# Kernel optimization log

Measured on AMD Instinct MI355X. Metric: run time of the kernel, lower is better.

## Reference

```python
import jax, jax.numpy as jnp
import numpy as np
import math

TEXT_EMBEDDING_DIM = 768.0
SEQ = 81
DIM = 64
B, H = 256, 16


def setup_inputs() -> dict:
    key = jax.random.key(0)
    kq, kk, kv, ke = jax.random.split(key, 4)
    Q = jax.random.normal(kq, (B, H, SEQ, DIM), dtype=jnp.float32)
    K = jax.random.normal(kk, (B, H, SEQ, DIM), dtype=jnp.float32)
    V = jax.random.normal(kv, (B, H, SEQ, DIM), dtype=jnp.float32)
    emb_table = jax.random.normal(ke, (2 * SEQ + 1, DIM), dtype=jnp.float32)
    return {"Q": Q, "K": K, "V": V, "emb_table": emb_table, "use_causal": 1}


def reference(Q, K, V, emb_table, use_causal):
    S = Q.shape[-2]
    # relative index matrix: rel[i, j] = (S - 1 + i) - j, in [0, 2S-2]
    rel = jnp.arange(S - 1, 2 * S - 1)[:, None] - jnp.arange(S)  # [S, S] int
    emb = emb_table[rel]  # [S, S, d]
    # QK^T plus learned relative-position bias
    eij = jnp.einsum('bhid,bhjd->bhij', Q, K) + jnp.einsum('bhid,ijd->bhij', Q, emb)
    attn = eij / math.sqrt(TEXT_EMBEDDING_DIM)  # note: sqrt(768), not sqrt(dim), per source
    if use_causal:
        i = jnp.arange(S)[:, None]
        j = jnp.arange(S)
        mask = jnp.where(i >= j, 0.0, -1000000000.0).astype(attn.dtype)  # [S, S]
        attn = attn + mask
    attn = jax.nn.softmax(attn, axis=-1)
    return jnp.einsum('bhij,bhjd->bhid', attn, V)
```

## Files before the change

kernel.cpp:

```cpp
#include <hip/hip_runtime.h>
#include <hip/hip_bf16.h>

#define SEQ 81
#define DIM 64
#define NT  384
#define NW  6
#define LDK 68
#define LDV 100
#define LDP 100

typedef short bf16x8 __attribute__((ext_vector_type(8)));
typedef short bf16x4 __attribute__((ext_vector_type(4)));
typedef float f32x4  __attribute__((ext_vector_type(4)));

static constexpr float kS2 = 0.0520587716f;

__device__ __forceinline__ short f2bf(float f) {
    __hip_bfloat16 h = __float2bfloat16(f);
    return __builtin_bit_cast(short, h);
}
__device__ __forceinline__ float bf2f(short h) {
    unsigned u = ((unsigned)(unsigned short)h) << 16;
    return __builtin_bit_cast(float, u);
}
__device__ __forceinline__ bf16x8 cat8(bf16x4 a, bf16x4 b) {
    bf16x8 r;
    r[0]=a[0]; r[1]=a[1]; r[2]=a[2]; r[3]=a[3];
    r[4]=b[0]; r[5]=b[1]; r[6]=b[2]; r[7]=b[3];
    return r;
}

__global__ void emb_cvt_kernel(const float* __restrict__ in, short* __restrict__ out, int n) {
    int i = blockIdx.x * 256 + threadIdx.x;
    if (i < n) out[i] = f2bf(in[i]);
}

__global__ __launch_bounds__(NT, 8)
void rpsa_kernel(const float* __restrict__ Q, const float* __restrict__ K,
                 const float* __restrict__ V, const short* __restrict__ embw,
                 const int* __restrict__ ucp, float* __restrict__ out)
{
    extern __shared__ char smraw[];
    short* sVt = (short*)smraw;
    short* sK  = (short*)(smraw + 12800);
    short* sP  = (short*)(smraw + 12800);

    const int tid = threadIdx.x;
    const size_t base = (size_t)blockIdx.x * (SEQ * DIM);
    const int uc = ucp[0];
    const int w  = tid >> 6, L = tid & 63;
    const int lr = L & 15,  lg = L >> 4;
    const int iRow = 16*w + lr;

    bf16x8 aq0, aq1;
    {
        const int qrow = (iRow < SEQ) ? iRow : (SEQ - 1);
        const float* qp = Q + base + qrow*DIM + 8*lg;
        const f32x4 q0 = *(const f32x4*)(qp);
        const f32x4 q1 = *(const f32x4*)(qp + 4);
        const f32x4 q2 = *(const f32x4*)(qp + 32);
        const f32x4 q3 = *(const f32x4*)(qp + 36);
        #pragma unroll
        for (int t = 0; t < 4; ++t) {
            aq0[t]   = f2bf(q0[t]*kS2);
            aq0[4+t] = f2bf(q1[t]*kS2);
            aq1[t]   = f2bf(q2[t]*kS2);
            aq1[4+t] = f2bf(q3[t]*kS2);
        }
    }

    for (int u = tid; u < 96 * DIM / 8; u += NT) {
        const int row = u >> 3, so = (u & 7) * 8;
        bf16x4 lo = {0,0,0,0}, hi = {0,0,0,0};
        if (row < SEQ) {
            const f32x4 k0 = *(const f32x4*)(K + base + row*DIM + so);
            const f32x4 k1 = *(const f32x4*)(K + base + row*DIM + so + 4);
            #pragma unroll
            for (int t = 0; t < 4; ++t) { lo[t] = f2bf(k0[t]); hi[t] = f2bf(k1[t]); }
        }
        *(bf16x4*)(sK + row*LDK + so)     = lo;
        *(bf16x4*)(sK + row*LDK + so + 4) = hi;
    }
    {
        const int j4 = tid >> 4;
        const int d4 = tid & 15;
        f32x4 rw[4];
        #pragma unroll
        for (int e = 0; e < 4; ++e) {
            const int j = 4*j4 + e;
            rw[e] = (j < SEQ) ? *(const f32x4*)(V + base + j*DIM + 4*d4)
                              : (f32x4){0.f,0.f,0.f,0.f};
        }
        #pragma unroll
        for (int c = 0; c < 4; ++c) {
            const int d = 4*d4 + c;
            bf16x4 pv = { f2bf(rw[0][c]), f2bf(rw[1][c]), f2bf(rw[2][c]), f2bf(rw[3][c]) };
            *(bf16x4*)(sVt + d*LDV + 4*j4) = pv;
        }
    }

    bf16x4 qe[NW];
    #pragma unroll
    for (int nt2 = 0; nt2 < NW; ++nt2) {
        if (nt2 > w) continue;
        int erow = 80 + 16*nt2 + lr;
        if (erow > 2*SEQ) erow = 2*SEQ;
        bf16x8 e0 = *(const bf16x8*)(embw + erow*DIM + 8*lg);
        bf16x8 e1 = *(const bf16x8*)(embw + erow*DIM + 32 + 8*lg);
        f32x4 a = {0.f,0.f,0.f,0.f};
        a = __builtin_amdgcn_mfma_f32_16x16x32_bf16(e0, aq0, a, 0, 0, 0);
        a = __builtin_amdgcn_mfma_f32_16x16x32_bf16(e1, aq1, a, 0, 0, 0);
        bf16x4 p = { f2bf(a[0]), f2bf(a[1]), f2bf(a[2]), f2bf(a[3]) };
        qe[nt2] = p;
    }
    __syncthreads();

    f32x4 accs[NW] = {};
    const int ntEnd = uc ? w : (NW - 1);
    #pragma unroll
    for (int nt = 0; nt < NW; ++nt) {
        if (nt > ntEnd) continue;
        const int kr = 16*nt + lr;
        bf16x8 b0 = cat8(*(const bf16x4*)(sK + kr*LDK + 8*lg),
                         *(const bf16x4*)(sK + kr*LDK + 8*lg + 4));
        bf16x8 b1 = cat8(*(const bf16x4*)(sK + kr*LDK + 32 + 8*lg),
                         *(const bf16x4*)(sK + kr*LDK + 32 + 8*lg + 4));
        f32x4 a = accs[nt];
        a = __builtin_amdgcn_mfma_f32_16x16x32_bf16(b0, aq0, a, 0, 0, 0);
        a = __builtin_amdgcn_mfma_f32_16x16x32_bf16(b1, aq1, a, 0, 0, 0);
        accs[nt] = a;
    }
    __syncthreads();

    #pragma unroll
    for (int nt2 = 0; nt2 < NW; ++nt2) {
        if (nt2 > w) continue;
        #pragma unroll
        for (int r = 0; r < 4; ++r) {
            const int j = 16*(w - nt2) + lr - 4*lg - r;
            if (j >= 0) sP[iRow*LDP + j] = qe[nt2][r];
        }
    }
    if (!uc) {
        #pragma unroll
        for (int nt2 = 0; nt2 < NW - 1; ++nt2) {
            if (nt2 < w) continue;
            const int erow = 16*nt2 + lr;
            bf16x8 e0 = *(const bf16x8*)(embw + erow*DIM + 8*lg);
            bf16x8 e1 = *(const bf16x8*)(embw + erow*DIM + 32 + 8*lg);
            f32x4 a = {0.f,0.f,0.f,0.f};
            a = __builtin_amdgcn_mfma_f32_16x16x32_bf16(e0, aq0, a, 0, 0, 0);
            a = __builtin_amdgcn_mfma_f32_16x16x32_bf16(e1, aq1, a, 0, 0, 0);
            #pragma unroll
            for (int r = 0; r < 4; ++r) {
                const int rel = 16*nt2 + 4*lg + r;
                if (rel >= iRow) sP[iRow*LDP + (80 + iRow - rel)] = f2bf(a[r]);
            }
        }
    }

    const int jmax = uc ? ((iRow < SEQ-1) ? iRow : SEQ-1) : (SEQ-1);
    float sum = 0.f;
    #pragma unroll
    for (int nt = 0; nt < NW; ++nt) {
        short* slot = sP + iRow*LDP + 16*nt + 4*lg;
        if (nt <= ntEnd) {
            bf16x4 bias = *(const bf16x4*)(slot);
            bf16x4 p;
            #pragma unroll
            for (int r = 0; r < 4; ++r) {
                const int j = 16*nt + 4*lg + r;
                const float x = accs[nt][r] + bf2f(bias[r]);
                const float e = (j <= jmax) ? exp2f(x) : 0.f;
                sum += e;
                p[r] = f2bf(e);
            }
            *(bf16x4*)(slot) = p;
        } else {
            *(bf16x4*)(slot) = (bf16x4){0,0,0,0};
        }
    }
    sum += __shfl_xor(sum, 16);
    sum += __shfl_xor(sum, 32);
    const float inv = 1.f / sum;

    bf16x8 ap0, ap1, ap2;
    {
        ap0 = cat8(*(const bf16x4*)(sP + iRow*LDP + 8*lg),
                   *(const bf16x4*)(sP + iRow*LDP + 8*lg + 4));
        ap1 = cat8(*(const bf16x4*)(sP + iRow*LDP + 32 + 8*lg),
                   *(const bf16x4*)(sP + iRow*LDP + 32 + 8*lg + 4));
        ap2 = cat8(*(const bf16x4*)(sP + iRow*LDP + 64 + 8*lg),
                   *(const bf16x4*)(sP + iRow*LDP + 64 + 8*lg + 4));
    }
    #pragma unroll
    for (int nt = 0; nt < 4; ++nt) {
        const int d = 16*nt + lr;
        bf16x8 b0 = cat8(*(const bf16x4*)(sVt + d*LDV + 8*lg),
                         *(const bf16x4*)(sVt + d*LDV + 8*lg + 4));
        bf16x8 b1 = cat8(*(const bf16x4*)(sVt + d*LDV + 32 + 8*lg),
                         *(const bf16x4*)(sVt + d*LDV + 32 + 8*lg + 4));
        bf16x8 b2 = cat8(*(const bf16x4*)(sVt + d*LDV + 64 + 8*lg),
                         *(const bf16x4*)(sVt + d*LDV + 64 + 8*lg + 4));
        f32x4 a = {0.f,0.f,0.f,0.f};
        a = __builtin_amdgcn_mfma_f32_16x16x32_bf16(b0, ap0, a, 0, 0, 0);
        a = __builtin_amdgcn_mfma_f32_16x16x32_bf16(b1, ap1, a, 0, 0, 0);
        a = __builtin_amdgcn_mfma_f32_16x16x32_bf16(b2, ap2, a, 0, 0, 0);
        if (iRow < SEQ) {
            f32x4 o = { a[0]*inv, a[1]*inv, a[2]*inv, a[3]*inv };
            *(f32x4*)(out + base + iRow*DIM + 16*nt + 4*lg) = o;
        }
    }
}

extern "C" void kernel_launch(void* const* d_in, const int* in_sizes, int n_in,
                              void* d_out, int out_size, void* d_ws, size_t ws_size,
                              hipStream_t stream) {
    const float* Q   = (const float*)d_in[0];
    const float* K   = (const float*)d_in[1];
    const float* V   = (const float*)d_in[2];
    const float* emb = (const float*)d_in[3];
    const int*   uc  = (const int*)d_in[4];
    float* out = (float*)d_out;

    const int nbh   = in_sizes[0] / (SEQ * DIM);
    const int n_emb = in_sizes[3];

    short* embw = (short*)d_ws;
    emb_cvt_kernel<<<(n_emb + 255) / 256, 256, 0, stream>>>(emb, embw, n_emb);

    const size_t smem = 32000;
    hipFuncSetAttribute(reinterpret_cast<const void*>(rpsa_kernel),
                        hipFuncAttributeMaxDynamicSharedMemorySize, (int)smem);
    rpsa_kernel<<<nbh, NT, smem, stream>>>(Q, K, V, embw, uc, out);
}
```

Before: 83.85 us.

## Load K directly into MFMA registers, drop K smem staging and a barrier

K is now read from global memory straight into MFMA operand registers and converted to bf16 in registers, instead of being staged through shared memory. This removes the K staging loop and one of the two __syncthreads. sP gets its own shared-memory region, LDV/LDP padding becomes 102, and bias scores are written to sP as soon as they are computed. The PV stage also skips k-slices above the causal limit for each wave. The tradeoff is that K rows are loaded redundantly by different waves, which adds global/L2 traffic in exchange for less LDS work and synchronisation.

```diff
diff --git a/kernel.cpp b/kernel.cpp
--- a/kernel.cpp
+++ b/kernel.cpp
@@ -5,9 +5,8 @@
 #define DIM 64
 #define NT  384
 #define NW  6
-#define LDK 68
-#define LDV 100
-#define LDP 100
+#define LDV 102
+#define LDP 102
 
 typedef short bf16x8 __attribute__((ext_vector_type(8)));
 typedef short bf16x4 __attribute__((ext_vector_type(4)));
@@ -42,8 +41,7 @@
 {
     extern __shared__ char smraw[];
     short* sVt = (short*)smraw;
-    short* sK  = (short*)(smraw + 12800);
-    short* sP  = (short*)(smraw + 12800);
+    short* sP  = (short*)(smraw + 13056);
 
     const int tid = threadIdx.x;
     const size_t base = (size_t)blockIdx.x * (SEQ * DIM);
@@ -51,6 +49,24 @@
     const int w  = tid >> 6, L = tid & 63;
     const int lr = L & 15,  lg = L >> 4;
     const int iRow = 16*w + lr;
+
+    {
+        const int j4 = tid >> 4;
+        const int d4 = tid & 15;
+        f32x4 rw[4];
+        #pragma unroll
+        for (int e = 0; e < 4; ++e) {
+            const int j = 4*j4 + e;
+            rw[e] = (j < SEQ) ? *(const f32x4*)(V + base + j*DIM + 4*d4)
+                              : (f32x4){0.f,0.f,0.f,0.f};
+        }
+        #pragma unroll
+        for (int c = 0; c < 4; ++c) {
+            const int d = 4*d4 + c;
+            bf16x4 pv = { f2bf(rw[0][c]), f2bf(rw[1][c]), f2bf(rw[2][c]), f2bf(rw[3][c]) };
+            *(bf16x4*)(sVt + d*LDV + 4*j4) = pv;
+        }
+    }
 
     bf16x8 aq0, aq1;
     {
@@ -69,37 +85,6 @@
         }
     }
 
-    for (int u = tid; u < 96 * DIM / 8; u += NT) {
-        const int row = u >> 3, so = (u & 7) * 8;
-        bf16x4 lo = {0,0,0,0}, hi = {0,0,0,0};
-        if (row < SEQ) {
-            const f32x4 k0 = *(const f32x4*)(K + base + row*DIM + so);
-            const f32x4 k1 = *(const f32x4*)(K + base + row*DIM + so + 4);
-            #pragma unroll
-            for (int t = 0; t < 4; ++t) { lo[t] = f2bf(k0[t]); hi[t] = f2bf(k1[t]); }
-        }
-        *(bf16x4*)(sK + row*LDK + so)     = lo;
-        *(bf16x4*)(sK + row*LDK + so + 4) = hi;
-    }
-    {
-        const int j4 = tid >> 4;
-        const int d4 = tid & 15;
-        f32x4 rw[4];
-        #pragma unroll
-        for (int e = 0; e < 4; ++e) {
-            const int j = 4*j4 + e;
-            rw[e] = (j < SEQ) ? *(const f32x4*)(V + base + j*DIM + 4*d4)
-                              : (f32x4){0.f,0.f,0.f,0.f};
-        }
-        #pragma unroll
-        for (int c = 0; c < 4; ++c) {
-            const int d = 4*d4 + c;
-            bf16x4 pv = { f2bf(rw[0][c]), f2bf(rw[1][c]), f2bf(rw[2][c]), f2bf(rw[3][c]) };
-            *(bf16x4*)(sVt + d*LDV + 4*j4) = pv;
-        }
-    }
-
-    bf16x4 qe[NW];
     #pragma unroll
     for (int nt2 = 0; nt2 < NW; ++nt2) {
         if (nt2 > w) continue;
@@ -110,35 +95,10 @@
         f32x4 a = {0.f,0.f,0.f,0.f};
         a = __builtin_amdgcn_mfma_f32_16x16x32_bf16(e0, aq0, a, 0, 0, 0);
         a = __builtin_amdgcn_mfma_f32_16x16x32_bf16(e1, aq1, a, 0, 0, 0);
-        bf16x4 p = { f2bf(a[0]), f2bf(a[1]), f2bf(a[2]), f2bf(a[3]) };
-        qe[nt2] = p;
-    }
-    __syncthreads();
-
-    f32x4 accs[NW] = {};
-    const int ntEnd = uc ? w : (NW - 1);
-    #pragma unroll
-    for (int nt = 0; nt < NW; ++nt) {
-        if (nt > ntEnd) continue;
-        const int kr = 16*nt + lr;
-        bf16x8 b0 = cat8(*(const bf16x4*)(sK + kr*LDK + 8*lg),
-                         *(const bf16x4*)(sK + kr*LDK + 8*lg + 4));
-        bf16x8 b1 = cat8(*(const bf16x4*)(sK + kr*LDK + 32 + 8*lg),
-                         *(const bf16x4*)(sK + kr*LDK + 32 + 8*lg + 4));
-        f32x4 a = accs[nt];
-        a = __builtin_amdgcn_mfma_f32_16x16x32_bf16(b0, aq0, a, 0, 0, 0);
-        a = __builtin_amdgcn_mfma_f32_16x16x32_bf16(b1, aq1, a, 0, 0, 0);
-        accs[nt] = a;
-    }
-    __syncthreads();
-
-    #pragma unroll
-    for (int nt2 = 0; nt2 < NW; ++nt2) {
-        if (nt2 > w) continue;
         #pragma unroll
         for (int r = 0; r < 4; ++r) {
             const int j = 16*(w - nt2) + lr - 4*lg - r;
-            if (j >= 0) sP[iRow*LDP + j] = qe[nt2][r];
+            if (j >= 0) sP[iRow*LDP + j] = f2bf(a[r]);
         }
     }
     if (!uc) {
@@ -157,6 +117,30 @@
                 if (rel >= iRow) sP[iRow*LDP + (80 + iRow - rel)] = f2bf(a[r]);
             }
         }
+    }
+
+    f32x4 accs[NW] = {};
+    const int ntEnd = uc ? w : (NW - 1);
+    #pragma unroll
+    for (int nt = 0; nt < NW; ++nt) {
+        if (nt > ntEnd) continue;
+        const int kr0 = 16*nt + lr;
+        const int kr  = (kr0 < SEQ) ? kr0 : (SEQ - 1);
+        const float* kp = K + base + kr*DIM + 8*lg;
+        const f32x4 k0 = *(const f32x4*)(kp);
+        const f32x4 k1 = *(const f32x4*)(kp + 4);
+        const f32x4 k2 = *(const f32x4*)(kp + 32);
+        const f32x4 k3 = *(const f32x4*)(kp + 36);
+        bf16x8 b0, b1;
+        #pragma unroll
+        for (int t = 0; t < 4; ++t) {
+            b0[t] = f2bf(k0[t]); b0[4+t] = f2bf(k1[t]);
+            b1[t] = f2bf(k2[t]); b1[4+t] = f2bf(k3[t]);
+        }
+        f32x4 a = accs[nt];
+        a = __builtin_amdgcn_mfma_f32_16x16x32_bf16(b0, aq0, a, 0, 0, 0);
+        a = __builtin_amdgcn_mfma_f32_16x16x32_bf16(b1, aq1, a, 0, 0, 0);
+        accs[nt] = a;
     }
 
     const int jmax = uc ? ((iRow < SEQ-1) ? iRow : SEQ-1) : (SEQ-1);
@@ -184,28 +168,33 @@
     sum += __shfl_xor(sum, 32);
     const float inv = 1.f / sum;
 
+    __syncthreads();
+
+    const int nks = uc ? ((w >> 1) + 1) : 3;
     bf16x8 ap0, ap1, ap2;
-    {
-        ap0 = cat8(*(const bf16x4*)(sP + iRow*LDP + 8*lg),
-                   *(const bf16x4*)(sP + iRow*LDP + 8*lg + 4));
-        ap1 = cat8(*(const bf16x4*)(sP + iRow*LDP + 32 + 8*lg),
-                   *(const bf16x4*)(sP + iRow*LDP + 32 + 8*lg + 4));
-        ap2 = cat8(*(const bf16x4*)(sP + iRow*LDP + 64 + 8*lg),
-                   *(const bf16x4*)(sP + iRow*LDP + 64 + 8*lg + 4));
-    }
+    ap0 = cat8(*(const bf16x4*)(sP + iRow*LDP + 8*lg),
+               *(const bf16x4*)(sP + iRow*LDP + 8*lg + 4));
+    ap1 = cat8(*(const bf16x4*)(sP + iRow*LDP + 32 + 8*lg),
+               *(const bf16x4*)(sP + iRow*LDP + 32 + 8*lg + 4));
+    ap2 = cat8(*(const bf16x4*)(sP + iRow*LDP + 64 + 8*lg),
+               *(const bf16x4*)(sP + iRow*LDP + 64 + 8*lg + 4));
     #pragma unroll
     for (int nt = 0; nt < 4; ++nt) {
         const int d = 16*nt + lr;
+        f32x4 a = {0.f,0.f,0.f,0.f};
         bf16x8 b0 = cat8(*(const bf16x4*)(sVt + d*LDV + 8*lg),
                          *(const bf16x4*)(sVt + d*LDV + 8*lg + 4));
-        bf16x8 b1 = cat8(*(const bf16x4*)(sVt + d*LDV + 32 + 8*lg),
-                         *(const bf16x4*)(sVt + d*LDV + 32 + 8*lg + 4));
-        bf16x8 b2 = cat8(*(const bf16x4*)(sVt + d*LDV + 64 + 8*lg),
-                         *(const bf16x4*)(sVt + d*LDV + 64 + 8*lg + 4));
-        f32x4 a = {0.f,0.f,0.f,0.f};
         a = __builtin_amdgcn_mfma_f32_16x16x32_bf16(b0, ap0, a, 0, 0, 0);
-        a = __builtin_amdgcn_mfma_f32_16x16x32_bf16(b1, ap1, a, 0, 0, 0);
-        a = __builtin_amdgcn_mfma_f32_16x16x32_bf16(b2, ap2, a, 0, 0, 0);
+        if (nks > 1) {
+            bf16x8 b1 = cat8(*(const bf16x4*)(sVt + d*LDV + 32 + 8*lg),
+                             *(const bf16x4*)(sVt + d*LDV + 32 + 8*lg + 4));
+            a = __builtin_amdgcn_mfma_f32_16x16x32_bf16(b1, ap1, a, 0, 0, 0);
+        }
+        if (nks > 2) {
+            bf16x8 b2 = cat8(*(const bf16x4*)(sVt + d*LDV + 64 + 8*lg),
+                             *(const bf16x4*)(sVt + d*LDV + 64 + 8*lg + 4));
+            a = __builtin_amdgcn_mfma_f32_16x16x32_bf16(b2, ap2, a, 0, 0, 0);
+        }
         if (iRow < SEQ) {
             f32x4 o = { a[0]*inv, a[1]*inv, a[2]*inv, a[3]*inv };
             *(f32x4*)(out + base + iRow*DIM + 16*nt + 4*lg) = o;
@@ -229,7 +218,7 @@
     short* embw = (short*)d_ws;
     emb_cvt_kernel<<<(n_emb + 255) / 256, 256, 0, stream>>>(emb, embw, n_emb);
 
-    const size_t smem = 32000;
+    const size_t smem = 32640;
     hipFuncSetAttribute(reinterpret_cast<const void*>(rpsa_kernel),
                         hipFuncAttributeMaxDynamicSharedMemorySize, (int)smem);
     rpsa_kernel<<<nbh, NT, smem, stream>>>(Q, K, V, embw, uc, out);
```

Measured after the change: 150.9 us. +80.0%, slower.

## Fuse embedding conversion into main kernel and skip masked PV k-steps

Applied to the files above, without the earlier changes.

Removes the separate fp32-to-bf16 embedding conversion kernel and launch; the attention kernel now reads fp32 embedding rows directly and converts them in registers. Under causal masking, each wave skips the PV MFMA k-slices (and their LDS loads) that lie entirely in the masked region. The V and P LDS row strides change from 100 to 102, presumably to reduce bank conflicts, which makes shared memory slightly larger. In exchange, each block does redundant embedding conversion and twice as many global bytes per embedding load, and there is a wave-dependent branch.

```diff
diff --git a/kernel.cpp b/kernel.cpp
--- a/kernel.cpp
+++ b/kernel.cpp
@@ -6,8 +6,8 @@
 #define NT  384
 #define NW  6
 #define LDK 68
-#define LDV 100
-#define LDP 100
+#define LDV 102
+#define LDP 102
 
 typedef short bf16x8 __attribute__((ext_vector_type(8)));
 typedef short bf16x4 __attribute__((ext_vector_type(4)));
@@ -29,21 +29,22 @@
     r[4]=b[0]; r[5]=b[1]; r[6]=b[2]; r[7]=b[3];
     return r;
 }
-
-__global__ void emb_cvt_kernel(const float* __restrict__ in, short* __restrict__ out, int n) {
-    int i = blockIdx.x * 256 + threadIdx.x;
-    if (i < n) out[i] = f2bf(in[i]);
+__device__ __forceinline__ bf16x8 cvt8(f32x4 a, f32x4 b) {
+    bf16x8 r;
+    #pragma unroll
+    for (int t = 0; t < 4; ++t) { r[t] = f2bf(a[t]); r[4+t] = f2bf(b[t]); }
+    return r;
 }
 
 __global__ __launch_bounds__(NT, 8)
 void rpsa_kernel(const float* __restrict__ Q, const float* __restrict__ K,
-                 const float* __restrict__ V, const short* __restrict__ embw,
+                 const float* __restrict__ V, const float* __restrict__ emb,
                  const int* __restrict__ ucp, float* __restrict__ out)
 {
     extern __shared__ char smraw[];
     short* sVt = (short*)smraw;
-    short* sK  = (short*)(smraw + 12800);
-    short* sP  = (short*)(smraw + 12800);
+    short* sK  = (short*)(smraw + 13056);
+    short* sP  = (short*)(smraw + 13056);
 
     const int tid = threadIdx.x;
     const size_t base = (size_t)blockIdx.x * (SEQ * DIM);
@@ -56,17 +57,8 @@
     {
         const int qrow = (iRow < SEQ) ? iRow : (SEQ - 1);
         const float* qp = Q + base + qrow*DIM + 8*lg;
-        const f32x4 q0 = *(const f32x4*)(qp);
-        const f32x4 q1 = *(const f32x4*)(qp + 4);
-        const f32x4 q2 = *(const f32x4*)(qp + 32);
-        const f32x4 q3 = *(const f32x4*)(qp + 36);
-        #pragma unroll
-        for (int t = 0; t < 4; ++t) {
-            aq0[t]   = f2bf(q0[t]*kS2);
-            aq0[4+t] = f2bf(q1[t]*kS2);
-            aq1[t]   = f2bf(q2[t]*kS2);
-            aq1[4+t] = f2bf(q3[t]*kS2);
-        }
+        aq0 = cvt8(*(const f32x4*)(qp)      * kS2, *(const f32x4*)(qp + 4)  * kS2);
+        aq1 = cvt8(*(const f32x4*)(qp + 32) * kS2, *(const f32x4*)(qp + 36) * kS2);
     }
 
     for (int u = tid; u < 96 * DIM / 8; u += NT) {
@@ -105,8 +97,9 @@
         if (nt2 > w) continue;
         int erow = 80 + 16*nt2 + lr;
         if (erow > 2*SEQ) erow = 2*SEQ;
-        bf16x8 e0 = *(const bf16x8*)(embw + erow*DIM + 8*lg);
-        bf16x8 e1 = *(const bf16x8*)(embw + erow*DIM + 32 + 8*lg);
+        const float* ep = emb + erow*DIM + 8*lg;
+        bf16x8 e0 = cvt8(*(const f32x4*)(ep),      *(const f32x4*)(ep + 4));
+        bf16x8 e1 = cvt8(*(const f32x4*)(ep + 32), *(const f32x4*)(ep + 36));
         f32x4 a = {0.f,0.f,0.f,0.f};
         a = __builtin_amdgcn_mfma_f32_16x16x32_bf16(e0, aq0, a, 0, 0, 0);
         a = __builtin_amdgcn_mfma_f32_16x16x32_bf16(e1, aq1, a, 0, 0, 0);
@@ -146,8 +139,9 @@
         for (int nt2 = 0; nt2 < NW - 1; ++nt2) {
             if (nt2 < w) continue;
             const int erow = 16*nt2 + lr;
-            bf16x8 e0 = *(const bf16x8*)(embw + erow*DIM + 8*lg);
-            bf16x8 e1 = *(const bf16x8*)(embw + erow*DIM + 32 + 8*lg);
+            const float* ep = emb + erow*DIM + 8*lg;
+            bf16x8 e0 = cvt8(*(const f32x4*)(ep),      *(const f32x4*)(ep + 4));
+            bf16x8 e1 = cvt8(*(const f32x4*)(ep + 32), *(const f32x4*)(ep + 36));
             f32x4 a = {0.f,0.f,0.f,0.f};
             a = __builtin_amdgcn_mfma_f32_16x16x32_bf16(e0, aq0, a, 0, 0, 0);
             a = __builtin_amdgcn_mfma_f32_16x16x32_bf16(e1, aq1, a, 0, 0, 0);
@@ -184,28 +178,33 @@
     sum += __shfl_xor(sum, 32);
     const float inv = 1.f / sum;
 
+    const int nks = uc ? ((w >> 1) + 1) : 3;
     bf16x8 ap0, ap1, ap2;
-    {
-        ap0 = cat8(*(const bf16x4*)(sP + iRow*LDP + 8*lg),
-                   *(const bf16x4*)(sP + iRow*LDP + 8*lg + 4));
+    ap0 = cat8(*(const bf16x4*)(sP + iRow*LDP + 8*lg),
+               *(const bf16x4*)(sP + iRow*LDP + 8*lg + 4));
+    if (nks > 1)
         ap1 = cat8(*(const bf16x4*)(sP + iRow*LDP + 32 + 8*lg),
                    *(const bf16x4*)(sP + iRow*LDP + 32 + 8*lg + 4));
+    if (nks > 2)
         ap2 = cat8(*(const bf16x4*)(sP + iRow*LDP + 64 + 8*lg),
                    *(const bf16x4*)(sP + iRow*LDP + 64 + 8*lg + 4));
-    }
     #pragma unroll
     for (int nt = 0; nt < 4; ++nt) {
         const int d = 16*nt + lr;
+        f32x4 a = {0.f,0.f,0.f,0.f};
         bf16x8 b0 = cat8(*(const bf16x4*)(sVt + d*LDV + 8*lg),
                          *(const bf16x4*)(sVt + d*LDV + 8*lg + 4));
-        bf16x8 b1 = cat8(*(const bf16x4*)(sVt + d*LDV + 32 + 8*lg),
-                         *(const bf16x4*)(sVt + d*LDV + 32 + 8*lg + 4));
-        bf16x8 b2 = cat8(*(const bf16x4*)(sVt + d*LDV + 64 + 8*lg),
-                         *(const bf16x4*)(sVt + d*LDV + 64 + 8*lg + 4));
-        f32x4 a = {0.f,0.f,0.f,0.f};
         a = __builtin_amdgcn_mfma_f32_16x16x32_bf16(b0, ap0, a, 0, 0, 0);
-        a = __builtin_amdgcn_mfma_f32_16x16x32_bf16(b1, ap1, a, 0, 0, 0);
-        a = __builtin_amdgcn_mfma_f32_16x16x32_bf16(b2, ap2, a, 0, 0, 0);
+        if (nks > 1) {
+            bf16x8 b1 = cat8(*(const bf16x4*)(sVt + d*LDV + 32 + 8*lg),
+                             *(const bf16x4*)(sVt + d*LDV + 32 + 8*lg + 4));
+            a = __builtin_amdgcn_mfma_f32_16x16x32_bf16(b1, ap1, a, 0, 0, 0);
+        }
+        if (nks > 2) {
+            bf16x8 b2 = cat8(*(const bf16x4*)(sVt + d*LDV + 64 + 8*lg),
+                             *(const bf16x4*)(sVt + d*LDV + 64 + 8*lg + 4));
+            a = __builtin_amdgcn_mfma_f32_16x16x32_bf16(b2, ap2, a, 0, 0, 0);
+        }
         if (iRow < SEQ) {
             f32x4 o = { a[0]*inv, a[1]*inv, a[2]*inv, a[3]*inv };
             *(f32x4*)(out + base + iRow*DIM + 16*nt + 4*lg) = o;
@@ -223,14 +222,10 @@
     const int*   uc  = (const int*)d_in[4];
     float* out = (float*)d_out;
 
-    const int nbh   = in_sizes[0] / (SEQ * DIM);
-    const int n_emb = in_sizes[3];
-
-    short* embw = (short*)d_ws;
-    emb_cvt_kernel<<<(n_emb + 255) / 256, 256, 0, stream>>>(emb, embw, n_emb);
-
-    const size_t smem = 32000;
+    const int nbh = in_sizes[0] / (SEQ * DIM);
+
+    const size_t smem = 32640;
     hipFuncSetAttribute(reinterpret_cast<const void*>(rpsa_kernel),
                         hipFuncAttributeMaxDynamicSharedMemorySize, (int)smem);
-    rpsa_kernel<<<nbh, NT, smem, stream>>>(Q, K, V, embw, uc, out);
-}
+    rpsa_kernel<<<nbh, NT, smem, stream>>>(Q, K, V, emb, uc, out);
+}
```

Result: slower. 118.5 us (+41.3%).
